# Kernel tuning notes

Hardware: AMD Instinct MI355X
Metric: run time of the kernel (lower is better)

## Reference

```python
import jax, jax.numpy as jnp
import numpy as np

B, SQ, SK, H, NH = 8, 1024, 1024, 512, 4
D = H // NH
MASK_FILL = -2.0 ** 32 + 1
LN_EPS = 1e-5


def setup_inputs() -> dict:
    key = jax.random.key(0)
    ks = jax.random.split(key, 9)
    memory = jax.random.normal(ks[0], (B, SK, H), dtype=jnp.float32)
    decoder_input = jax.random.normal(ks[1], (B, SQ, H), dtype=jnp.float32)
    mask = jax.random.randint(ks[2], (B, SQ, SK), 0, 2).astype(bool)
    query_mask = jax.random.randint(ks[3], (B, SQ), 0, 2).astype(jnp.float32)
    # Linear weights stored torch-style as (out_dim, in_dim), xavier-ish scale
    scale = 1.0 / np.sqrt(H)
    Wk = jax.random.uniform(ks[4], (H, H), jnp.float32, -scale, scale)
    Wv = jax.random.uniform(ks[5], (H, H), jnp.float32, -scale, scale)
    Wq = jax.random.uniform(ks[6], (H, H), jnp.float32, -scale, scale)
    gamma = jnp.ones((H,), jnp.float32)
    beta = jnp.zeros((H,), jnp.float32)
    return {"memory": memory, "decoder_input": decoder_input, "mask": mask,
            "query_mask": query_mask, "Wk": Wk, "Wv": Wv, "Wq": Wq,
            "gamma": gamma, "beta": beta}


def reference(memory, decoder_input, mask, query_mask, Wk, Wv, Wq, gamma, beta):
    # projections (torch Linear: y = x @ W.T), split into heads
    k = jnp.einsum('bsh,oh->bso', memory, Wk).reshape(B, SK, NH, D)
    v = jnp.einsum('bsh,oh->bso', memory, Wv).reshape(B, SK, NH, D)
    q = jnp.einsum('bsh,oh->bso', decoder_input, Wq).reshape(B, SQ, NH, D)
    # scaled dot-product scores: [h, B, Sq, Sk]
    scores = jnp.einsum('bqhd,bkhd->hbqk', q, k) / jnp.sqrt(jnp.float32(D))
    scores = jnp.where(mask[None], jnp.float32(MASK_FILL), scores)
    attn = jax.nn.softmax(scores, axis=-1)
    # post-softmax multiplicative query mask
    attn = attn * query_mask[None, :, :, None]
    out = jnp.einsum('hbqk,bkhd->bqhd', attn, v).reshape(B, SQ, H)
    # residual + LayerNorm
    x = out + decoder_input
    mu = jnp.mean(x, axis=-1, keepdims=True)
    var = jnp.mean((x - mu) ** 2, axis=-1, keepdims=True)
    result = (x - mu) * jax.lax.rsqrt(var + LN_EPS) * gamma + beta
    # attn returned in torch layout [h*B, Sq, Sk]
    return result, attn.reshape(NH * B, SQ, SK)
```

## Files before the change

kernel.cpp:

```cpp
#include <hip/hip_runtime.h>
#include <hip/hip_bf16.h>
#include <stdint.h>

#define NB 8
#define NSQ 1024
#define NSK 1024
#define NHID 512
#define NHEAD 4
#define NDH 128

typedef __attribute__((ext_vector_type(8))) short short8;
typedef __attribute__((ext_vector_type(4))) float f32x4;
typedef __attribute__((ext_vector_type(4))) int i32x4;

__device__ __forceinline__ unsigned short f2b(float f) {
  unsigned int u = __builtin_bit_cast(unsigned int, f);
  u = u + 0x7FFFu + ((u >> 16) & 1u);
  return (unsigned short)(u >> 16);
}

__device__ __forceinline__ float b2f(unsigned short s) {
  unsigned int u = ((unsigned int)s) << 16;
  return __builtin_bit_cast(float, u);
}

__device__ __forceinline__ short8 pack8v(f32x4 a, f32x4 b) {
  short8 o;
  o[0] = (short)f2b(a.x); o[1] = (short)f2b(a.y);
  o[2] = (short)f2b(a.z); o[3] = (short)f2b(a.w);
  o[4] = (short)f2b(b.x); o[5] = (short)f2b(b.y);
  o[6] = (short)f2b(b.z); o[7] = (short)f2b(b.w);
  return o;
}

__device__ __forceinline__ void gl2lds16(const unsigned short* g, unsigned short* l) {
  __builtin_amdgcn_global_load_lds(
      (const __attribute__((address_space(1))) void*)g,
      (__attribute__((address_space(3))) void*)l, 16, 0, 0);
}

__global__ __launch_bounds__(256) void cvt_pack(
    const float* __restrict__ dec, const float* __restrict__ mem,
    const float* __restrict__ Wq, const float* __restrict__ Wk,
    const float* __restrict__ Wv, const int* __restrict__ mask,
    unsigned short* __restrict__ decB, unsigned short* __restrict__ memB,
    unsigned short* __restrict__ WB, unsigned int* __restrict__ mw) {
  const int bid = blockIdx.x, tid = threadIdx.x;
  if (bid >= 4480) {
    int w = (bid - 4480) * 256 + tid;
    const int* src = mask + (size_t)w * 32;
    unsigned int bits = 0;
#pragma unroll
    for (int j = 0; j < 32; j += 4) {
      i32x4 v = *(const i32x4*)(src + j);
      bits |= (v.x ? 1u << j : 0u) | (v.y ? 1u << (j + 1) : 0u) |
              (v.z ? 1u << (j + 2) : 0u) | (v.w ? 1u << (j + 3) : 0u);
    }
    int row = w >> 5, wi = w & 31;
    mw[(size_t)row * 32 + ((wi & 3) * 8 + (wi >> 2))] = bits;
    return;
  }
  const float* src;
  unsigned short* dst;
  int base_row;
  if (bid < 2048) { src = dec; dst = decB; base_row = bid * 4; }
  else if (bid < 4096) { src = mem; dst = memB; base_row = (bid - 2048) * 4; }
  else {
    int w = bid - 4096;
    int wi = w >> 7;
    src = (wi == 0) ? Wq : (wi == 1) ? Wk : Wv;
    dst = WB + (size_t)wi * 262144;
    base_row = (w & 127) * 4;
  }
  const int row = base_row + (tid >> 6);
  const int kpos = (tid & 63) * 8;
  const float* s = src + (size_t)row * 512 + kpos;
  f32x4 a0 = *(const f32x4*)s;
  f32x4 a1 = *(const f32x4*)(s + 4);
  const int mt = row >> 7, kt = kpos >> 6, pr = row & 127, c = (kpos & 63) >> 3;
  *(short8*)&dst[(size_t)(mt * 8 + kt) * 8192 + pr * 64 + ((c ^ (pr & 7)) * 8)] =
      pack8v(a0, a1);
}

__global__ __launch_bounds__(256) void proj_gemm_all(
    const unsigned short* __restrict__ decB, const unsigned short* __restrict__ memB,
    const unsigned short* __restrict__ WB, unsigned short* __restrict__ Cb) {
  __shared__ unsigned short tA[2][8192];
  __shared__ unsigned short tB[2][8192];
  const int z = blockIdx.z;
  const int mt = blockIdx.x, h = blockIdx.y;
  const unsigned short* A = (z == 0) ? decB : memB;
  const unsigned short* W = WB + (size_t)z * 262144;
  unsigned short* C = Cb + (size_t)z * 4194304;
  const bool tr = (z == 2);
  const int tid = threadIdx.x, lane = tid & 63, wave = tid >> 6;
  const int wm = (wave & 1) * 64, wn = (wave >> 1) * 64;
  const int r15 = lane & 15, hi = lane >> 4;

  auto stage = [&](int kt, int sel) {
#pragma unroll
    for (int i = 0; i < 4; ++i) {
      int ci = i * 4 + wave;
      gl2lds16(A + (size_t)(mt * 8 + kt) * 8192 + ci * 512 + lane * 8,
               &tA[sel][ci * 512 + lane * 8]);
      gl2lds16(W + (size_t)(h * 8 + kt) * 8192 + ci * 512 + lane * 8,
               &tB[sel][ci * 512 + lane * 8]);
    }
  };

  f32x4 acc[4][4];
  for (int i = 0; i < 4; ++i)
    for (int j = 0; j < 4; ++j) acc[i][j] = (f32x4){0.f, 0.f, 0.f, 0.f};

  stage(0, 0);
  __syncthreads();
  for (int kt = 0; kt < 8; ++kt) {
    const int sel = kt & 1;
    if (kt < 7) stage(kt + 1, sel ^ 1);
    __builtin_amdgcn_s_setprio(1);
#pragma unroll
    for (int kk = 0; kk < 2; ++kk) {
      short8 af[4], bf[4];
#pragma unroll
      for (int mi = 0; mi < 4; ++mi) {
        int row = wm + mi * 16 + r15;
        af[mi] = *(short8*)&tA[sel][row * 64 + (((kk * 4 + hi) ^ (row & 7)) * 8)];
      }
#pragma unroll
      for (int ni = 0; ni < 4; ++ni) {
        int row = wn + ni * 16 + r15;
        bf[ni] = *(short8*)&tB[sel][row * 64 + (((kk * 4 + hi) ^ (row & 7)) * 8)];
      }
#pragma unroll
      for (int mi = 0; mi < 4; ++mi)
#pragma unroll
        for (int ni = 0; ni < 4; ++ni)
          acc[mi][ni] = __builtin_amdgcn_mfma_f32_16x16x32_bf16(
              af[mi], bf[ni], acc[mi][ni], 0, 0, 0);
    }
    __builtin_amdgcn_s_setprio(0);
    __syncthreads();
  }

#pragma unroll
  for (int mi = 0; mi < 4; ++mi)
#pragma unroll
    for (int ni = 0; ni < 4; ++ni)
#pragma unroll
      for (int r = 0; r < 4; ++r) {
        int m = mt * 128 + wm + mi * 16 + hi * 4 + r;
        int d = wn + ni * 16 + r15;
        int bq = m >> 10, q = m & 1023, t = q >> 7, pr = q & 127;
        size_t pbase = (size_t)((bq * 4 + h) * 8 + t) * 16384;
        unsigned short v = f2b(acc[mi][ni][r]);
        if (!tr)
          C[pbase + pr * 128 + (((d >> 3) ^ (pr & 7)) * 8) + (d & 7)] = v;
        else
          C[pbase + d * 128 + (((pr >> 3) ^ (d & 7)) * 8) + (pr & 7)] = v;
      }
}

__global__ __launch_bounds__(512, 4) void attn_s_kernel(
    const unsigned short* __restrict__ Qb, const unsigned short* __restrict__ Kb,
    const unsigned int* __restrict__ maskp, const float* __restrict__ qmask,
    float* __restrict__ attn) {
  __shared__ unsigned short tQ[32 * 128];
  __shared__ unsigned short buf0[128 * 128];
  __shared__ unsigned short buf1[128 * 128];
  __shared__ float redsum[32][8];
  const int L = blockIdx.x;
  const int r_ = L & 7;
  const int j_ = L >> 3;
  const int qt = j_ & 31;
  const int hb = (j_ >> 5) * 8 + r_;
  const int h = hb >> 3, b = hb & 7;
  const int q0 = qt * 32;
  const int tid = threadIdx.x;
  const int lane = tid & 63, wave = tid >> 6;
  const int r15 = lane & 15, hi = lane >> 4;

  auto stageK = [&](int t, unsigned short* buf) {
    const unsigned short* p = Kb + (size_t)((b * 4 + h) * 8 + t) * 16384;
#pragma unroll
    for (int i = 0; i < 4; ++i) {
      int ci = i * 8 + wave;
      gl2lds16(p + ci * 512 + lane * 8, buf + ci * 512 + lane * 8);
    }
  };
  {
    const unsigned short* p =
        Qb + (size_t)((b * 4 + h) * 8 + (q0 >> 7)) * 16384 + (q0 & 127) * 128;
    gl2lds16(p + wave * 512 + lane * 8, tQ + wave * 512 + lane * 8);
  }
  stageK(0, buf0);
  __syncthreads();

  f32x4 acc[2][8];
#pragma unroll
  for (int g = 0; g < 2; ++g)
#pragma unroll
    for (int t = 0; t < 8; ++t) acc[g][t] = (f32x4){0.f, 0.f, 0.f, 0.f};

#pragma unroll
  for (int t = 0; t < 8; ++t) {
    if (t < 7) stageK(t + 1, (t & 1) ? buf0 : buf1);
    const unsigned short* kb = (t & 1) ? buf1 : buf0;
    __builtin_amdgcn_s_setprio(1);
#pragma unroll
    for (int ks = 0; ks < 4; ++ks) {
      const int sw = ((ks * 4 + hi) ^ (r15 & 7)) * 8;
      short8 bk = *(const short8*)&kb[(wave * 16 + r15) * 128 + sw];
#pragma unroll
      for (int g = 0; g < 2; ++g) {
        short8 aqv = *(const short8*)&tQ[(g * 16 + r15) * 128 + sw];
        acc[g][t] = __builtin_amdgcn_mfma_f32_16x16x32_bf16(aqv, bk, acc[g][t], 0, 0, 0);
      }
    }
    __builtin_amdgcn_s_setprio(0);
    __syncthreads();
  }

  const float isd = 0.08838834764831845f;
  const int sh = (wave & 1) * 16 + r15;
#pragma unroll
  for (int g = 0; g < 2; ++g)
#pragma unroll
    for (int r = 0; r < 4; ++r) {
      const unsigned int* mrow =
          maskp + ((size_t)(b * NSQ) + q0 + g * 16 + hi * 4 + r) * 32 + (wave >> 1) * 8;
      uint4 wa = *(const uint4*)mrow;
      uint4 wb = *(const uint4*)(mrow + 4);
      unsigned int mw8[8] = {wa.x, wa.y, wa.z, wa.w, wb.x, wb.y, wb.z, wb.w};
      float sm = 0.f;
#pragma unroll
      for (int t = 0; t < 8; ++t) {
        unsigned int bit = (mw8[t] >> sh) & 1u;
        float s = acc[g][t][r] * isd;
        float e = __expf(bit ? -4294967296.0f : s);
        acc[g][t][r] = e;
        sm += e;
      }
      sm += __shfl_xor(sm, 1);
      sm += __shfl_xor(sm, 2);
      sm += __shfl_xor(sm, 4);
      sm += __shfl_xor(sm, 8);
      if (r15 == 0) redsum[g * 16 + hi * 4 + r][wave] = sm;
    }
  __syncthreads();
#pragma unroll
  for (int g = 0; g < 2; ++g)
#pragma unroll
    for (int r = 0; r < 4; ++r) {
      float4 a = *(float4*)&redsum[g * 16 + hi * 4 + r][0];
      float4 c = *(float4*)&redsum[g * 16 + hi * 4 + r][4];
      float sum = (a.x + a.y + a.z + a.w) + (c.x + c.y + c.z + c.w);
      float scl = qmask[b * NSQ + q0 + g * 16 + hi * 4 + r] / sum;
#pragma unroll
      for (int t = 0; t < 8; ++t) acc[g][t][r] *= scl;
    }

#pragma unroll
  for (int g = 0; g < 2; ++g) {
    float* abase =
        attn + ((size_t)hb * NSQ + q0 + g * 16 + hi * 4) * NSK + wave * 16 + r15;
#pragma unroll
    for (int t = 0; t < 8; ++t)
#pragma unroll
      for (int r = 0; r < 4; ++r) abase[(r << 10) + t * 128] = acc[g][t][r];
  }
}

__global__ __launch_bounds__(256) void pv_gemm(const float* __restrict__ attn,
                                               const unsigned short* __restrict__ Vtb,
                                               unsigned short* __restrict__ outh) {
  __shared__ unsigned short tA[64 * 128];
  __shared__ unsigned short tB[128 * 128];
  const int L = blockIdx.x;
  const int r_ = L & 7, q_ = (L >> 3) & 15, s_ = L >> 7;
  const int hb = s_ * 8 + r_;
  const int h = hb >> 3, b = hb & 7;
  const int m0 = q_ * 64;
  const int tid = threadIdx.x;
  const int lane = tid & 63;
  const int wave = tid >> 6;
  const int wn = wave * 32;
  const int r15 = lane & 15, hi = lane >> 4;
  const float* Abase = attn + (size_t)hb * NSQ * NSK;

  f32x4 acc[4][2];
  for (int i = 0; i < 4; ++i)
    for (int j = 0; j < 2; ++j) acc[i][j] = (f32x4){0.f, 0.f, 0.f, 0.f};

  for (int kt = 0; kt < 8; ++kt) {
    {
      const unsigned short* p = Vtb + (size_t)((b * 4 + h) * 8 + kt) * 16384;
#pragma unroll
      for (int i = 0; i < 8; ++i) {
        int ci = i * 4 + wave;
        gl2lds16(p + ci * 512 + lane * 8, tB + ci * 512 + lane * 8);
      }
    }
#pragma unroll
    for (int it = 0; it < 4; ++it) {
      int idx = it * 256 + tid;
      int row = idx >> 4, c = idx & 15;
      const float* sa = Abase + (size_t)(m0 + row) * NSK + kt * 128 + c * 8;
      f32x4 a0 = *(const f32x4*)sa;
      f32x4 a1 = *(const f32x4*)(sa + 4);
      *(short8*)&tA[row * 128 + ((c ^ (row & 7)) * 8)] = pack8v(a0, a1);
    }
    __syncthreads();
    __builtin_amdgcn_s_setprio(1);
#pragma unroll
    for (int ks = 0; ks < 4; ++ks) {
      short8 af[4], bf[2];
#pragma unroll
      for (int mi = 0; mi < 4; ++mi) {
        int row = mi * 16 + r15;
        af[mi] = *(short8*)&tA[row * 128 + (((ks * 4 + hi) ^ (row & 7)) * 8)];
      }
#pragma unroll
      for (int ni = 0; ni < 2; ++ni) {
        int row = wn + ni * 16 + r15;
        bf[ni] = *(short8*)&tB[row * 128 + (((ks * 4 + hi) ^ (row & 7)) * 8)];
      }
#pragma unroll
      for (int mi = 0; mi < 4; ++mi)
#pragma unroll
        for (int ni = 0; ni < 2; ++ni)
          acc[mi][ni] = __builtin_amdgcn_mfma_f32_16x16x32_bf16(
              af[mi], bf[ni], acc[mi][ni], 0, 0, 0);
    }
    __builtin_amdgcn_s_setprio(0);
    __syncthreads();
  }
#pragma unroll
  for (int mi = 0; mi < 4; ++mi)
#pragma unroll
    for (int ni = 0; ni < 2; ++ni)
#pragma unroll
      for (int r = 0; r < 4; ++r) {
        int m = m0 + mi * 16 + hi * 4 + r;
        int n = wn + ni * 16 + r15;
        outh[(size_t)(b * NSQ + m) * NHID + h * NDH + n] = f2b(acc[mi][ni][r]);
      }
}

__global__ __launch_bounds__(256) void ln_kernel(const unsigned short* __restrict__ outh,
                                                 const float* __restrict__ dec,
                                                 const float* __restrict__ gamma,
                                                 const float* __restrict__ beta,
                                                 float* __restrict__ result) {
  const int tid = threadIdx.x;
  const int lane = tid & 63, wave = tid >> 6;
  const size_t row = (size_t)blockIdx.x * 4 + wave;
  const unsigned short* xr = outh + row * NHID;
  const float* dr = dec + row * NHID;
  float v[8];
  float s = 0.f;
  short8 xv = *(const short8*)(xr + lane * 8);
  for (int j = 0; j < 2; ++j) {
    float4 d = *(const float4*)(dr + lane * 8 + j * 4);
    v[j * 4 + 0] = b2f((unsigned short)xv[j * 4 + 0]) + d.x;
    v[j * 4 + 1] = b2f((unsigned short)xv[j * 4 + 1]) + d.y;
    v[j * 4 + 2] = b2f((unsigned short)xv[j * 4 + 2]) + d.z;
    v[j * 4 + 3] = b2f((unsigned short)xv[j * 4 + 3]) + d.w;
  }
  for (int j = 0; j < 8; ++j) s += v[j];
  for (int off = 32; off > 0; off >>= 1) s += __shfl_xor(s, off);
  float mu = s * (1.f / 512.f);
  float s2 = 0.f;
  for (int j = 0; j < 8; ++j) {
    float d = v[j] - mu;
    s2 += d * d;
  }
  for (int off = 32; off > 0; off >>= 1) s2 += __shfl_xor(s2, off);
  float rstd = rsqrtf(s2 * (1.f / 512.f) + 1e-5f);
  float* out = result + row * NHID;
  for (int j = 0; j < 2; ++j) {
    float4 g = *(const float4*)(gamma + lane * 8 + j * 4);
    float4 bt = *(const float4*)(beta + lane * 8 + j * 4);
    float4 o;
    o.x = (v[j * 4 + 0] - mu) * rstd * g.x + bt.x;
    o.y = (v[j * 4 + 1] - mu) * rstd * g.y + bt.y;
    o.z = (v[j * 4 + 2] - mu) * rstd * g.z + bt.z;
    o.w = (v[j * 4 + 3] - mu) * rstd * g.w + bt.w;
    *(float4*)(out + lane * 8 + j * 4) = o;
  }
}

extern "C" void kernel_launch(void* const* d_in, const int* in_sizes, int n_in,
                              void* d_out, int out_size, void* d_ws, size_t ws_size,
                              hipStream_t stream) {
  const float* memory = (const float*)d_in[0];
  const float* dec = (const float*)d_in[1];
  const int* mask = (const int*)d_in[2];
  const float* qmask = (const float*)d_in[3];
  const float* Wk = (const float*)d_in[4];
  const float* Wv = (const float*)d_in[5];
  const float* Wq = (const float*)d_in[6];
  const float* gamma = (const float*)d_in[7];
  const float* beta = (const float*)d_in[8];

  char* ws = (char*)d_ws;
  unsigned short* decBb = (unsigned short*)(ws + 0);
  unsigned short* memBb = (unsigned short*)(ws + 8388608);
  unsigned short* outh = (unsigned short*)(ws + 0);
  unsigned short* WB = (unsigned short*)(ws + 16777216);
  unsigned short* QKVb = (unsigned short*)(ws + 18350080);
  unsigned int* maskw = (unsigned int*)(ws + 43515904);

  unsigned short* Qb = QKVb;
  unsigned short* Kb = QKVb + 4194304;
  unsigned short* Vtb = QKVb + 8388608;

  float* resultp = (float*)d_out;
  float* attnp = resultp + 4194304;

  cvt_pack<<<dim3(5504), dim3(256), 0, stream>>>(dec, memory, Wq, Wk, Wv, mask,
                                                 decBb, memBb, WB, maskw);
  proj_gemm_all<<<dim3(64, 4, 3), dim3(256), 0, stream>>>(decBb, memBb, WB, QKVb);

  attn_s_kernel<<<dim3(1024), dim3(512), 0, stream>>>(Qb, Kb, maskw, qmask, attnp);
  pv_gemm<<<dim3(512), dim3(256), 0, stream>>>(attnp, Vtb, outh);
  ln_kernel<<<dim3(2048), dim3(256), 0, stream>>>(outh, dec, gamma, beta, resultp);
}
```

Measured before the change: 114.8 us.

## Emit bf16 swizzled probability copy for PV GEMM and stream fp32 attn stores

The softmax kernel now writes, alongside the fp32 attention output, a bf16 copy of the probabilities in a pre-tiled, XOR-swizzled layout that matches the PV GEMM's LDS tiles. The PV GEMM then loads its A operand with direct global-to-LDS copies instead of reading fp32 rows and converting them in registers. The fp32 output stores are marked nontemporal. This halves the bytes the PV GEMM reads, but adds an extra bf16 write stream of 2-byte scattered stores to the softmax kernel and needs more workspace.

```diff
diff --git a/kernel.cpp b/kernel.cpp
--- a/kernel.cpp
+++ b/kernel.cpp
@@ -163,7 +163,7 @@
 __global__ __launch_bounds__(512, 4) void attn_s_kernel(
     const unsigned short* __restrict__ Qb, const unsigned short* __restrict__ Kb,
     const unsigned int* __restrict__ maskp, const float* __restrict__ qmask,
-    float* __restrict__ attn) {
+    float* __restrict__ attn, unsigned short* __restrict__ Pb) {
   __shared__ unsigned short tQ[32 * 128];
   __shared__ unsigned short buf0[128 * 128];
   __shared__ unsigned short buf1[128 * 128];
@@ -259,18 +259,28 @@
       for (int t = 0; t < 8; ++t) acc[g][t][r] *= scl;
     }
 
+  const int pc = wave * 2 + (r15 >> 3);
 #pragma unroll
   for (int g = 0; g < 2; ++g) {
     float* abase =
         attn + ((size_t)hb * NSQ + q0 + g * 16 + hi * 4) * NSK + wave * 16 + r15;
+    const int qrow0 = (qt & 1) * 32 + g * 16 + hi * 4;
+    unsigned short* pbase =
+        Pb + ((size_t)(hb * 16 + (qt >> 1)) * 8) * 8192 + (size_t)qrow0 * 128 +
+        (r15 & 7);
 #pragma unroll
     for (int t = 0; t < 8; ++t)
 #pragma unroll
-      for (int r = 0; r < 4; ++r) abase[(r << 10) + t * 128] = acc[g][t][r];
-  }
-}
-
-__global__ __launch_bounds__(256) void pv_gemm(const float* __restrict__ attn,
+      for (int r = 0; r < 4; ++r) {
+        float p = acc[g][t][r];
+        __builtin_nontemporal_store(p, abase + (r << 10) + t * 128);
+        int row = qrow0 + r;
+        pbase[(size_t)t * 8192 + r * 128 + ((pc ^ (row & 7)) << 3)] = f2b(p);
+      }
+  }
+}
+
+__global__ __launch_bounds__(256) void pv_gemm(const unsigned short* __restrict__ Pb,
                                                const unsigned short* __restrict__ Vtb,
                                                unsigned short* __restrict__ outh) {
   __shared__ unsigned short tA[64 * 128];
@@ -285,7 +295,7 @@
   const int wave = tid >> 6;
   const int wn = wave * 32;
   const int r15 = lane & 15, hi = lane >> 4;
-  const float* Abase = attn + (size_t)hb * NSQ * NSK;
+  const unsigned short* Pbase = Pb + ((size_t)(hb * 16 + q_) * 8) * 8192;
 
   f32x4 acc[4][2];
   for (int i = 0; i < 4; ++i)
@@ -300,14 +310,13 @@
         gl2lds16(p + ci * 512 + lane * 8, tB + ci * 512 + lane * 8);
       }
     }
-#pragma unroll
-    for (int it = 0; it < 4; ++it) {
-      int idx = it * 256 + tid;
-      int row = idx >> 4, c = idx & 15;
-      const float* sa = Abase + (size_t)(m0 + row) * NSK + kt * 128 + c * 8;
-      f32x4 a0 = *(const f32x4*)sa;
-      f32x4 a1 = *(const f32x4*)(sa + 4);
-      *(short8*)&tA[row * 128 + ((c ^ (row & 7)) * 8)] = pack8v(a0, a1);
+    {
+      const unsigned short* p = Pbase + (size_t)kt * 8192;
+#pragma unroll
+      for (int i = 0; i < 4; ++i) {
+        int ci = i * 4 + wave;
+        gl2lds16(p + ci * 512 + lane * 8, tA + ci * 512 + lane * 8);
+      }
     }
     __syncthreads();
     __builtin_amdgcn_s_setprio(1);
@@ -409,6 +418,7 @@
   unsigned short* WB = (unsigned short*)(ws + 16777216);
   unsigned short* QKVb = (unsigned short*)(ws + 18350080);
   unsigned int* maskw = (unsigned int*)(ws + 43515904);
+  unsigned short* Pbuf = (unsigned short*)(ws + 44564480);
 
   unsigned short* Qb = QKVb;
   unsigned short* Kb = QKVb + 4194304;
@@ -421,7 +431,8 @@
                                                  decBb, memBb, WB, maskw);
   proj_gemm_all<<<dim3(64, 4, 3), dim3(256), 0, stream>>>(decBb, memBb, WB, QKVb);
 
-  attn_s_kernel<<<dim3(1024), dim3(512), 0, stream>>>(Qb, Kb, maskw, qmask, attnp);
-  pv_gemm<<<dim3(512), dim3(256), 0, stream>>>(attnp, Vtb, outh);
+  attn_s_kernel<<<dim3(1024), dim3(512), 0, stream>>>(Qb, Kb, maskw, qmask, attnp,
+                                                      Pbuf);
+  pv_gemm<<<dim3(512), dim3(256), 0, stream>>>(Pbuf, Vtb, outh);
   ln_kernel<<<dim3(2048), dim3(256), 0, stream>>>(outh, dec, gamma, beta, resultp);
 }
```

Result: slower. 123.5 us (+7.6%).
